# Performance work log

Measured on AMD Instinct MI355X. Metric: run time of the kernel, lower is better.

Reference implementation:

```python
import jax, jax.numpy as jnp
import numpy as np

B, S, C = 2, 2048, 1024          # batch, seq (= text_max_block_size), channels
H, D = 16, 64                    # num_heads, key_dim (C // H)
TEMP = 1e4                       # RoPE temperature
NEG_INF = -1e9


def rope(x):
    # x: [B, S, H, D]; interleaved-pair rotary embedding over sequence positions
    b, s, h, d = x.shape
    half = d // 2
    dim_t = TEMP ** (jnp.arange(half, dtype=jnp.float32) / half)      # [half]
    ang = jnp.arange(s, dtype=jnp.float32)[:, None] / dim_t            # [S, half]
    sin = jnp.sin(ang)[None, :, None, :]                               # [1,S,1,half]
    cos = jnp.cos(ang)[None, :, None, :]
    xr = x.reshape(b, s, h, half, 2)
    x1, x2 = xr[..., 0], xr[..., 1]
    out = jnp.stack([x1 * cos - x2 * sin, x2 * cos + x1 * sin], axis=-1)
    return out.reshape(b, s, h, d)


def setup_inputs() -> dict:
    key = jax.random.key(0)
    ks = jax.random.split(key, 5)
    w_scale = 0.02
    return {
        "x": jax.random.normal(ks[0], (B, S, C), jnp.float32),
        "w_qkv": jax.random.normal(ks[1], (C, 3 * C), jnp.float32) * w_scale,
        "q_bias": jax.random.normal(ks[2], (C,), jnp.float32) * w_scale,
        "v_bias": jax.random.normal(ks[3], (C,), jnp.float32) * w_scale,
        "w_out": jax.random.normal(ks[4], (C, C), jnp.float32) * w_scale,
    }


def reference(x, w_qkv, q_bias, v_bias, w_out):
    # fused QKV projection (no bias: qkv_bias=False)
    qkv = x @ w_qkv                                   # [B,S,3C]
    q, k, v = jnp.split(qkv, 3, axis=-1)
    # qv_bias=True: learnable bias on query and value only
    q = q + q_bias
    v = v + v_bias
    # inline RoPE on Q/K (PositionalEncodingFourierRot1D on [.., H, D/2, 2])
    q = rope(q.reshape(B, S, H, D))                   # [B,S,H,D]
    k = rope(k.reshape(B, S, H, D))
    v = v.reshape(B, S, H, D)
    scale = 1.0 / jnp.sqrt(jnp.float32(D))            # qk_scale <= 0 -> 1/sqrt(key_dim)
    scores = jnp.einsum("bqhd,bkhd->bhqk", q, k) * scale
    # CausalMask injected between scores and softmax
    causal = jnp.tril(jnp.ones((S, S), dtype=bool))
    scores = jnp.where(causal[None, None], scores, jnp.float32(NEG_INF))
    attn = jax.nn.softmax(scores, axis=-1)
    out = jnp.einsum("bhqk,bkhd->bqhd", attn, v).reshape(B, S, C)
    # output projection (return_weight=True, return_bias=False)
    return out @ w_out
```

## Files before the change

### kernel.cpp

```cpp
#include <hip/hip_runtime.h>
#include <stdint.h>

#define AS1 __attribute__((address_space(1)))
#define AS3 __attribute__((address_space(3)))

typedef __attribute__((ext_vector_type(8))) short bf16x8;
typedef __attribute__((ext_vector_type(4))) float f32x4;

__device__ __forceinline__ unsigned short f32_bf16(float f) {
  unsigned u = __float_as_uint(f);
  u += 0x7FFFu + ((u >> 16) & 1u);
  return (unsigned short)(u >> 16);
}

__device__ __forceinline__ void async_ld16(const unsigned short* g, unsigned short* l) {
  __builtin_amdgcn_global_load_lds((const AS1 void*)g, (AS3 void*)l, 16, 0, 0);
}

__device__ __forceinline__ void transpose_tile(const float* __restrict__ src,
                                               unsigned short* __restrict__ dst,
                                               int K, int N, int nt, int kt,
                                               unsigned short (*tile)[65]) {
  int t = threadIdx.x;
  #pragma unroll
  for (int i = 0; i < 16; ++i) {
    int idx = t + i * 256;
    int r = idx >> 6, c = idx & 63;
    tile[r][c] = f32_bf16(src[(size_t)(kt * 64 + r) * N + nt * 64 + c]);
  }
  __syncthreads();
  #pragma unroll
  for (int i = 0; i < 16; ++i) {
    int idx = t + i * 256;
    int r = idx >> 6, c = idx & 63;
    dst[(size_t)(nt * 64 + r) * K + kt * 64 + c] = tile[c][r];
  }
}

__global__ __launch_bounds__(256) void prep(const float* __restrict__ x,
                                            const float* __restrict__ w_qkv,
                                            const float* __restrict__ w_out,
                                            unsigned short* __restrict__ Xb,
                                            unsigned short* __restrict__ WqkvT,
                                            unsigned short* __restrict__ WoT,
                                            float2* __restrict__ ropeT) {
  __shared__ unsigned short tile[64][65];
  int bid = blockIdx.x;
  if (bid < 4096) {
    int i = bid * 256 + threadIdx.x;
    float4 v = ((const float4*)x)[i];
    ushort4 o;
    o.x = f32_bf16(v.x); o.y = f32_bf16(v.y); o.z = f32_bf16(v.z); o.w = f32_bf16(v.w);
    ((ushort4*)Xb)[i] = o;
  } else if (bid < 4864) {
    int b2 = bid - 4096;
    transpose_tile(w_qkv, WqkvT, 1024, 3072, b2 % 48, b2 / 48, tile);
  } else if (bid < 5120) {
    int b2 = bid - 4864;
    transpose_tile(w_out, WoT, 1024, 1024, b2 % 16, b2 / 16, tile);
  } else {
    int idx = (bid - 5120) * 256 + threadIdx.x;
    int s = idx >> 5, p = idx & 31;
    float invf = exp2f((float)p * (-13.287712379549449f / 32.f));
    float sn, cs;
    __sincosf((float)s * invf, &sn, &cs);
    ropeT[idx] = make_float2(cs, sn);
  }
}

template <int KDIM>
__device__ __forceinline__ void gemm_core(const unsigned short* __restrict__ A,
                                          const unsigned short* __restrict__ Bt,
                                          unsigned short* Als, unsigned short* Bls,
                                          int bm, int bn, f32x4 (&acc)[4][4]) {
  const int tid = threadIdx.x;
  const int w = tid >> 6, lane = tid & 63, quad = lane >> 4, l15 = lane & 15;
  const int wr = w >> 1, wc = w & 1;
  const int srow = lane >> 2, scol = (lane & 3) * 8;
  const unsigned short* Arow0 = A + (size_t)(bm * 128) * KDIM;
  const unsigned short* Brow0 = Bt + (size_t)(bn * 128) * KDIM;
  for (int k0 = 0; k0 < KDIM; k0 += 32) {
    __syncthreads();
    #pragma unroll
    for (int i = 0; i < 2; ++i) {
      int row = i * 64 + w * 16 + srow;
      async_ld16(Arow0 + (size_t)row * KDIM + k0 + scol, Als + i * 2048 + w * 512 + lane * 8);
      async_ld16(Brow0 + (size_t)row * KDIM + k0 + scol, Bls + i * 2048 + w * 512 + lane * 8);
    }
    __syncthreads();
    bf16x8 a[4], b[4];
    #pragma unroll
    for (int mi = 0; mi < 4; ++mi)
      a[mi] = *(const bf16x8*)(Als + (wr * 64 + mi * 16 + l15) * 32 + quad * 8);
    #pragma unroll
    for (int ni = 0; ni < 4; ++ni)
      b[ni] = *(const bf16x8*)(Bls + (wc * 64 + ni * 16 + l15) * 32 + quad * 8);
    #pragma unroll
    for (int mi = 0; mi < 4; ++mi)
      #pragma unroll
      for (int ni = 0; ni < 4; ++ni)
        acc[mi][ni] = __builtin_amdgcn_mfma_f32_16x16x32_bf16(a[mi], b[ni], acc[mi][ni], 0, 0, 0);
  }
}

__global__ __launch_bounds__(256, 3) void qkv_gemm(const unsigned short* __restrict__ Xb,
                                                   const unsigned short* __restrict__ WqkvT,
                                                   const float* __restrict__ qbias,
                                                   const float* __restrict__ vbias,
                                                   const float2* __restrict__ ropeT,
                                                   unsigned short* __restrict__ Qg,
                                                   unsigned short* __restrict__ Kg,
                                                   unsigned short* __restrict__ Vtg) {
  __shared__ unsigned short Als[128 * 32];
  __shared__ unsigned short Bls[128 * 32];
  __shared__ unsigned short Slds[4][64 * 72];
  f32x4 acc[4][4] = {};
  const int bn = blockIdx.x, bm = blockIdx.y;
  gemm_core<1024>(Xb, WqkvT, Als, Bls, bm, bn, acc);

  const int tid = threadIdx.x;
  const int w = tid >> 6, lane = tid & 63, quad = lane >> 4, l15 = lane & 15;
  const int wr = w >> 1, wc = w & 1;
  const int part = bn >> 3;
  const int cb = (bn & 7) * 128 + wc * 64;
  const int h = cb >> 6;
  const int m0 = bm * 128 + wr * 64;
  const int bb = m0 >> 11, s0 = m0 & 2047;
  unsigned short* Sw = Slds[w];

  if (part < 2) {
    const float qscale = (part == 0) ? 0.18033688011112042f : 1.f;
    #pragma unroll
    for (int ni = 0; ni < 4; ++ni) {
      int dd = ni * 16 + l15;
      float bias = (part == 0) ? qbias[cb + dd] : 0.f;
      float sgn = (dd & 1) ? 1.f : -1.f;
      const float2* tp = ropeT + (size_t)s0 * 32 + (dd >> 1);
      #pragma unroll
      for (int mi = 0; mi < 4; ++mi) {
        #pragma unroll
        for (int r = 0; r < 4; ++r) {
          int sl = mi * 16 + quad * 4 + r;
          float val = acc[mi][ni][r] + bias;
          float partner = __shfl_xor(val, 1);
          float2 cssn = tp[sl * 32];
          val = (val * cssn.x + sgn * partner * cssn.y) * qscale;
          Sw[sl * 72 + dd] = f32_bf16(val);
        }
      }
    }
    unsigned short* dstp = (part == 0) ? Qg : Kg;
    const size_t base = ((size_t)(bb * 16 + h) * 2048 + s0) * 64;
    #pragma unroll
    for (int it = 0; it < 8; ++it) {
      int row = it * 8 + (lane >> 3), off = (lane & 7) * 8;
      bf16x8 v = *(const bf16x8*)(Sw + row * 72 + off);
      *(bf16x8*)(dstp + base + (size_t)row * 64 + off) = v;
    }
  } else {
    #pragma unroll
    for (int ni = 0; ni < 4; ++ni) {
      int dd = ni * 16 + l15;
      float bias = vbias[cb + dd];
      #pragma unroll
      for (int mi = 0; mi < 4; ++mi)
        #pragma unroll
        for (int r = 0; r < 4; ++r) {
          int sl = mi * 16 + quad * 4 + r;
          Sw[sl * 68 + dd] = f32_bf16(acc[mi][ni][r] + bias);
        }
    }
    const size_t vbase = (size_t)(bb * 16 + h) * 64 * 2048 + s0;
    #pragma unroll 4
    for (int dd = 0; dd < 64; ++dd) {
      unsigned short v = Sw[lane * 68 + dd];
      Vtg[vbase + (size_t)dd * 2048 + lane] = v;
    }
  }
}

__global__ __launch_bounds__(256, 4) void attn_fwd(const unsigned short* __restrict__ Qg,
                                                   const unsigned short* __restrict__ Kg,
                                                   const unsigned short* __restrict__ Vtg,
                                                   unsigned short* __restrict__ Og) {
  __shared__ unsigned short Kls[2 * 128 * 32];
  __shared__ unsigned short Vls[4 * 64 * 32];
  __shared__ unsigned short Pls[4][2 * 16 * 32];
  const int bid = blockIdx.x;
  const int ix = bid >> 3;
  const int bh = ((bid & 7) << 2) + (ix & 3);
  const int s = ix >> 2;
  const int m = s & 7, t = s >> 3;
  const int qt = (t == 0) ? m : (t == 1) ? (31 - m) : (t == 2) ? (8 + m) : (23 - m);
  const int h = bh & 15, b = bh >> 4;
  const int tid = threadIdx.x;
  const int w = tid >> 6, lane = tid & 63, quad = lane >> 4, l15 = lane & 15;
  const unsigned short* Qb = Qg + (size_t)bh * 2048 * 64;
  const unsigned short* Kb = Kg + (size_t)bh * 2048 * 64;
  const unsigned short* Vb = Vtg + (size_t)bh * 64 * 2048;
  const int q0 = qt * 64 + w * 16;

  bf16x8 aq[2];
  #pragma unroll
  for (int ki = 0; ki < 2; ++ki)
    aq[ki] = *(const bf16x8*)(Qb + (size_t)(q0 + l15) * 64 + ki * 32 + quad * 8);

  f32x4 o[4] = {};
  float l_st[4] = {0.f, 0.f, 0.f, 0.f};

  unsigned short* Pw = Pls[w];
  const int nkt = (qt >> 1) + 1;

  for (int kt = 0; kt < nkt; ++kt) {
    __syncthreads();
    #pragma unroll
    for (int i = 0; i < 4; ++i) {
      int j = i * 4 + w;
      int kr = (j & 7) * 16 + (lane >> 2);
      int kc = (j >> 3) * 32 + (lane & 3) * 8;
      async_ld16(Kb + (size_t)(kt * 128 + kr) * 64 + kc, Kls + j * 512 + lane * 8);
      int dd = (j & 3) * 16 + (lane >> 2);
      int vc = (j >> 2) * 32 + (lane & 3) * 8;
      async_ld16(Vb + (size_t)dd * 2048 + kt * 128 + vc, Vls + j * 512 + lane * 8);
    }
    __syncthreads();

    f32x4 sc[8] = {};
    #pragma unroll
    for (int ki = 0; ki < 2; ++ki) {
      bf16x8 bk[8];
      #pragma unroll
      for (int ni = 0; ni < 8; ++ni)
        bk[ni] = *(const bf16x8*)(Kls + ki * 4096 + (ni * 16 + l15) * 32 + quad * 8);
      #pragma unroll
      for (int ni = 0; ni < 8; ++ni)
        sc[ni] = __builtin_amdgcn_mfma_f32_16x16x32_bf16(aq[ki], bk[ni], sc[ni], 0, 0, 0);
    }

    if (kt == (qt >> 1)) {
      #pragma unroll
      for (int r = 0; r < 4; ++r) {
        int row = q0 + quad * 4 + r;
        #pragma unroll
        for (int ni = 0; ni < 8; ++ni) {
          bool masked = (kt * 128 + ni * 16 + l15) > row;
          float pv = __builtin_amdgcn_exp2f(sc[ni][r] - 8.f);
          pv = masked ? 0.f : pv;
          sc[ni][r] = pv;
          l_st[r] += pv;
        }
      }
    } else {
      #pragma unroll
      for (int r = 0; r < 4; ++r)
        #pragma unroll
        for (int ni = 0; ni < 8; ++ni) {
          float pv = __builtin_amdgcn_exp2f(sc[ni][r] - 8.f);
          sc[ni][r] = pv;
          l_st[r] += pv;
        }
    }

    #pragma unroll
    for (int half = 0; half < 2; ++half) {
      #pragma unroll
      for (int nl = 0; nl < 4; ++nl) {
        int ck = ((nl & 1) << 1) | (l15 >> 3);
        int cs = ck ^ quad;
        #pragma unroll
        for (int r = 0; r < 4; ++r) {
          int rw = quad * 4 + r;
          Pw[(nl >> 1) * 512 + rw * 32 + cs * 8 + (l15 & 7)] =
              f32_bf16(sc[half * 4 + nl][r]);
        }
      }
      #pragma unroll
      for (int k4l = 0; k4l < 2; ++k4l) {
        int k4 = half * 2 + k4l;
        bf16x8 ap, bv[4];
        int csr = quad ^ ((l15 >> 2) & 3);
        ap = *(const bf16x8*)(Pw + k4l * 512 + l15 * 32 + csr * 8);
        #pragma unroll
        for (int di = 0; di < 4; ++di)
          bv[di] = *(const bf16x8*)(Vls + k4 * 2048 + (di * 16 + l15) * 32 + quad * 8);
        #pragma unroll
        for (int di = 0; di < 4; ++di)
          o[di] = __builtin_amdgcn_mfma_f32_16x16x32_bf16(ap, bv[di], o[di], 0, 0, 0);
      }
    }
  }

  #pragma unroll
  for (int r = 0; r < 4; ++r) {
    float s2 = l_st[r];
    s2 += __shfl_xor(s2, 1);
    s2 += __shfl_xor(s2, 2);
    s2 += __shfl_xor(s2, 4);
    s2 += __shfl_xor(s2, 8);
    l_st[r] = 1.f / s2;
  }
  #pragma unroll
  for (int r = 0; r < 4; ++r) {
    float inv = l_st[r];
    int sl = quad * 4 + r;
    #pragma unroll
    for (int di = 0; di < 4; ++di) {
      int ck = di * 2 + (l15 >> 3);
      int cs = ck ^ (sl & 7);
      Pw[sl * 64 + cs * 8 + (l15 & 7)] = f32_bf16(o[di][r] * inv);
    }
  }
  const size_t ob = ((size_t)(b * 2048 + q0)) * 1024 + h * 64;
  #pragma unroll
  for (int it = 0; it < 2; ++it) {
    int row = it * 8 + (lane >> 3);
    int cs = (lane & 7) ^ (row & 7);
    bf16x8 v = *(const bf16x8*)(Pw + row * 64 + cs * 8);
    *(bf16x8*)(Og + ob + (size_t)row * 1024 + (lane & 7) * 8) = v;
  }
}

__global__ __launch_bounds__(256, 2) void out_gemm(const unsigned short* __restrict__ Og,
                                                   const unsigned short* __restrict__ WoT,
                                                   float* __restrict__ Cout) {
  __shared__ unsigned short Als[128 * 32];
  __shared__ unsigned short Bls[128 * 32];
  f32x4 acc[4][4] = {};
  const int bn = blockIdx.x, bm = blockIdx.y;
  gemm_core<1024>(Og, WoT, Als, Bls, bm, bn, acc);
  const int tid = threadIdx.x;
  const int w = tid >> 6, lane = tid & 63, quad = lane >> 4, l15 = lane & 15;
  const int wr = w >> 1, wc = w & 1;
  #pragma unroll
  for (int mi = 0; mi < 4; ++mi)
    #pragma unroll
    for (int r = 0; r < 4; ++r) {
      int mm = bm * 128 + wr * 64 + mi * 16 + quad * 4 + r;
      #pragma unroll
      for (int ni = 0; ni < 4; ++ni) {
        int n = bn * 128 + wc * 64 + ni * 16 + l15;
        Cout[(size_t)mm * 1024 + n] = acc[mi][ni][r];
      }
    }
}

extern "C" void kernel_launch(void* const* d_in, const int* in_sizes, int n_in,
                              void* d_out, int out_size, void* d_ws, size_t ws_size,
                              hipStream_t stream) {
  const float* x      = (const float*)d_in[0];
  const float* w_qkv  = (const float*)d_in[1];
  const float* q_bias = (const float*)d_in[2];
  const float* v_bias = (const float*)d_in[3];
  const float* w_out  = (const float*)d_in[4];
  float* out = (float*)d_out;

  char* ws = (char*)d_ws;
  unsigned short* Xb    = (unsigned short*)(ws);
  unsigned short* WqkvT = (unsigned short*)(ws + (8u  << 20));
  unsigned short* WoT   = (unsigned short*)(ws + (14u << 20));
  unsigned short* Qg    = (unsigned short*)(ws + (16u << 20));
  unsigned short* Kg    = (unsigned short*)(ws + (24u << 20));
  unsigned short* Vtg   = (unsigned short*)(ws + (32u << 20));
  unsigned short* Og    = (unsigned short*)(ws + (40u << 20));
  float2* ropeT         = (float2*)(ws + (48u << 20));

  prep<<<5376, 256, 0, stream>>>(x, w_qkv, w_out, Xb, WqkvT, WoT, ropeT);
  qkv_gemm<<<dim3(24, 32), 256, 0, stream>>>(Xb, WqkvT, q_bias, v_bias, ropeT, Qg, Kg, Vtg);
  attn_fwd<<<1024, 256, 0, stream>>>(Qg, Kg, Vtg, Og);
  out_gemm<<<dim3(8, 32), 256, 0, stream>>>(Og, WoT, out);
}
```

Before: 184.0 us.

## Prefetch next K/V tile into registers during attention compute

Replaces the synchronous global-to-LDS async loads of each K/V tile with a register-staged prefetch. The next tile is loaded into registers while the current tile's QK and PV MFMAs run, then written to LDS at the top of the next iteration. This hides global load latency behind compute. In exchange it raises register pressure and adds a redundant load on the final iteration, and the LDS writes now go through VGPRs instead of the direct global_load_lds path.

```diff
diff --git a/kernel.cpp b/kernel.cpp
--- a/kernel.cpp
+++ b/kernel.cpp
@@ -211,19 +211,40 @@
   unsigned short* Pw = Pls[w];
   const int nkt = (qt >> 1) + 1;
 
+  const int j  = w;
+  bf16x8 kreg[4], vreg[4];
+  #pragma unroll
+  for (int i = 0; i < 4; ++i) {
+    int jj = i * 4 + w;
+    int kr = (jj & 7) * 16 + (lane >> 2);
+    int kc = (jj >> 3) * 32 + (lane & 3) * 8;
+    kreg[i] = *(const bf16x8*)(Kb + (size_t)kr * 64 + kc);
+    int dd = (jj & 3) * 16 + (lane >> 2);
+    int vc = (jj >> 2) * 32 + (lane & 3) * 8;
+    vreg[i] = *(const bf16x8*)(Vb + (size_t)dd * 2048 + vc);
+  }
+  (void)j;
+
   for (int kt = 0; kt < nkt; ++kt) {
+    #pragma unroll
+    for (int i = 0; i < 4; ++i) {
+      int jj = i * 4 + w;
+      *(bf16x8*)(Kls + jj * 512 + lane * 8) = kreg[i];
+      *(bf16x8*)(Vls + jj * 512 + lane * 8) = vreg[i];
+    }
     __syncthreads();
+
+    const int ktn = (kt + 1 < nkt) ? kt + 1 : kt;
     #pragma unroll
     for (int i = 0; i < 4; ++i) {
-      int j = i * 4 + w;
-      int kr = (j & 7) * 16 + (lane >> 2);
-      int kc = (j >> 3) * 32 + (lane & 3) * 8;
-      async_ld16(Kb + (size_t)(kt * 128 + kr) * 64 + kc, Kls + j * 512 + lane * 8);
-      int dd = (j & 3) * 16 + (lane >> 2);
-      int vc = (j >> 2) * 32 + (lane & 3) * 8;
-      async_ld16(Vb + (size_t)dd * 2048 + kt * 128 + vc, Vls + j * 512 + lane * 8);
-    }
-    __syncthreads();
+      int jj = i * 4 + w;
+      int kr = (jj & 7) * 16 + (lane >> 2);
+      int kc = (jj >> 3) * 32 + (lane & 3) * 8;
+      kreg[i] = *(const bf16x8*)(Kb + (size_t)(ktn * 128 + kr) * 64 + kc);
+      int dd = (jj & 3) * 16 + (lane >> 2);
+      int vc = (jj >> 2) * 32 + (lane & 3) * 8;
+      vreg[i] = *(const bf16x8*)(Vb + (size_t)dd * 2048 + ktn * 128 + vc);
+    }
 
     f32x4 sc[8] = {};
     #pragma unroll
@@ -288,6 +309,7 @@
           o[di] = __builtin_amdgcn_mfma_f32_16x16x32_bf16(ap, bv[di], o[di], 0, 0, 0);
       }
     }
+    __syncthreads();
   }
 
   #pragma unroll
```

New measurement: 184.3 us. No clear change (+0.2%).
